# Kernel optimization log

Measured on AMD Instinct MI355X. Metric: run time of the kernel, lower is better.

Reference implementation:

```python
import jax, jax.numpy as jnp
import numpy as np

IN_F = 4096
OUT_F = 4096
BATCH = 4096


def _dequantize(q, mn, mx):
    # Faithful to dequantize_to_float32: per-tensor affine using the *observed*
    # integer min/max of the stored tensor.
    q_min = q.min()
    q_max = q.max()
    scale = (mx - mn) / (q_max - q_min).astype(jnp.float32)
    return (q - q_min).astype(jnp.float32) * scale + mn


def setup_inputs() -> dict:
    key = jax.random.key(0)
    k1, k2, k3 = jax.random.split(key, 3)
    x = jax.random.normal(k1, (BATCH, IN_F), dtype=jnp.float32)
    # int8-valued weights/bias stored as int32 (same math; dequant uses tensor min/max)
    weight_q = jax.random.randint(k2, (OUT_F, IN_F), -128, 128, dtype=jnp.int32)
    bias_q = jax.random.randint(k3, (OUT_F,), -128, 128, dtype=jnp.int32)
    # per-tensor float range recorded at quantization time (original scales by 255 first,
    # so these ranges are on the scaled tensor; any floats work for correctness testing)
    weight_min = jnp.float32(-4.2)
    weight_max = jnp.float32(4.5)
    bias_min = jnp.float32(-1.3)
    bias_max = jnp.float32(1.1)
    return {
        "x": x,
        "weight_q": weight_q,
        "bias_q": bias_q,
        "weight_min": weight_min,
        "weight_max": weight_max,
        "bias_min": bias_min,
        "bias_max": bias_max,
    }


def reference(x, weight_q, bias_q, weight_min, weight_max, bias_min, bias_max):
    w = _dequantize(weight_q, weight_min, weight_max)   # [OUT_F, IN_F] fp32
    b = _dequantize(bias_q, bias_min, bias_max)         # [OUT_F] fp32
    # F.linear: x @ W^T + b
    return jnp.einsum("bi,oi->bo", x, w) + b
```

## Files before the change

kernel.cpp:

```cpp
#include <hip/hip_runtime.h>
#include <climits>

#define IN_F 4096
#define OUT_F 4096
#define BATCH 4096
#define NPART 1024

typedef __bf16 bf16x8 __attribute__((ext_vector_type(8)));
typedef float f32x4 __attribute__((ext_vector_type(4)));

__device__ __forceinline__ unsigned short f2bf_rne(float f) {
  unsigned int u = __float_as_uint(f);
  u += 0x7fffu + ((u >> 16) & 1u);
  return (unsigned short)(u >> 16);
}

__global__ __launch_bounds__(256) void k_conv(const float* __restrict__ x,
                                              const int* __restrict__ q,
                                              unsigned short* __restrict__ xb,
                                              unsigned short* __restrict__ qb,
                                              float* __restrict__ rowsum,
                                              int* __restrict__ pmin,
                                              int* __restrict__ pmax) {
  if (blockIdx.x < NPART) {
    const int n4 = (OUT_F * IN_F) / 4;
    const int stride = NPART * 256;
    int vmin = INT_MAX, vmax = INT_MIN;
    const int4* q4 = (const int4*)q;
    ushort4* qb4 = (ushort4*)qb;
    for (int i = blockIdx.x * 256 + threadIdx.x; i < n4; i += stride) {
      int4 v = q4[i];
      vmin = min(vmin, min(min(v.x, v.y), min(v.z, v.w)));
      vmax = max(vmax, max(max(v.x, v.y), max(v.z, v.w)));
      ushort4 h;
      h.x = f2bf_rne((float)v.x);
      h.y = f2bf_rne((float)v.y);
      h.z = f2bf_rne((float)v.z);
      h.w = f2bf_rne((float)v.w);
      qb4[i] = h;
    }
    for (int off = 32; off > 0; off >>= 1) {
      vmin = min(vmin, __shfl_down(vmin, off));
      vmax = max(vmax, __shfl_down(vmax, off));
    }
    __shared__ int rmin[4], rmax[4];
    const int wave = threadIdx.x >> 6;
    if ((threadIdx.x & 63) == 0) { rmin[wave] = vmin; rmax[wave] = vmax; }
    __syncthreads();
    if (threadIdx.x == 0) {
      pmin[blockIdx.x] = min(min(rmin[0], rmin[1]), min(rmin[2], rmin[3]));
      pmax[blockIdx.x] = max(max(rmax[0], rmax[1]), max(rmax[2], rmax[3]));
    }
  } else {
    const int wave = threadIdx.x >> 6;
    const int lane = threadIdx.x & 63;
    const int row = (blockIdx.x - NPART) * 4 + wave;
    const float4* xr = (const float4*)(x + (size_t)row * IN_F);
    ushort4* xbr = (ushort4*)(xb + (size_t)row * IN_F);
    float s = 0.f;
#pragma unroll
    for (int it = 0; it < IN_F / 4 / 64; ++it) {
      const int i = it * 64 + lane;
      float4 v = xr[i];
      s += (v.x + v.y) + (v.z + v.w);
      ushort4 h;
      h.x = f2bf_rne(v.x); h.y = f2bf_rne(v.y);
      h.z = f2bf_rne(v.z); h.w = f2bf_rne(v.w);
      xbr[i] = h;
    }
    for (int off = 32; off > 0; off >>= 1) s += __shfl_down(s, off);
    if (lane == 0) rowsum[row] = s;
  }
}

__global__ __launch_bounds__(256) void k_wmm(const int* __restrict__ q,
                                             int* __restrict__ pmin,
                                             int* __restrict__ pmax) {
  const int n4 = (OUT_F * IN_F) / 4;
  const int stride = gridDim.x * blockDim.x;
  int vmin = INT_MAX, vmax = INT_MIN;
  const int4* q4 = (const int4*)q;
  for (int i = blockIdx.x * blockDim.x + threadIdx.x; i < n4; i += stride) {
    int4 v = q4[i];
    vmin = min(vmin, min(min(v.x, v.y), min(v.z, v.w)));
    vmax = max(vmax, max(max(v.x, v.y), max(v.z, v.w)));
  }
  for (int off = 32; off > 0; off >>= 1) {
    vmin = min(vmin, __shfl_down(vmin, off));
    vmax = max(vmax, __shfl_down(vmax, off));
  }
  __shared__ int rmin[4], rmax[4];
  const int wave = threadIdx.x >> 6;
  if ((threadIdx.x & 63) == 0) { rmin[wave] = vmin; rmax[wave] = vmax; }
  __syncthreads();
  if (threadIdx.x == 0) {
    pmin[blockIdx.x] = min(min(rmin[0], rmin[1]), min(rmin[2], rmin[3]));
    pmax[blockIdx.x] = max(max(rmax[0], rmax[1]), max(rmax[2], rmax[3]));
  }
}

__global__ __launch_bounds__(256) void k_scal(const int* __restrict__ pmin,
                                              const int* __restrict__ pmax, int npart,
                                              const int* __restrict__ bq,
                                              const float* __restrict__ wmn,
                                              const float* __restrict__ wmx,
                                              const float* __restrict__ bmn,
                                              const float* __restrict__ bmx,
                                              float* __restrict__ scal) {
  int vmin = INT_MAX, vmax = INT_MIN;
  for (int i = threadIdx.x; i < npart; i += 256) {
    vmin = min(vmin, pmin[i]);
    vmax = max(vmax, pmax[i]);
  }
  int bmin = INT_MAX, bmaxv = INT_MIN;
  for (int i = threadIdx.x; i < OUT_F; i += 256) {
    int v = bq[i];
    bmin = min(bmin, v);
    bmaxv = max(bmaxv, v);
  }
  for (int off = 32; off > 0; off >>= 1) {
    vmin = min(vmin, __shfl_down(vmin, off));
    vmax = max(vmax, __shfl_down(vmax, off));
    bmin = min(bmin, __shfl_down(bmin, off));
    bmaxv = max(bmaxv, __shfl_down(bmaxv, off));
  }
  __shared__ int r[4][4];
  const int wave = threadIdx.x >> 6;
  if ((threadIdx.x & 63) == 0) {
    r[wave][0] = vmin; r[wave][1] = vmax; r[wave][2] = bmin; r[wave][3] = bmaxv;
  }
  __syncthreads();
  if (threadIdx.x == 0) {
    int qmin = min(min(r[0][0], r[1][0]), min(r[2][0], r[3][0]));
    int qmax = max(max(r[0][1], r[1][1]), max(r[2][1], r[3][1]));
    int qbmin = min(min(r[0][2], r[1][2]), min(r[2][2], r[3][2]));
    int qbmax = max(max(r[0][3], r[1][3]), max(r[2][3], r[3][3]));
    float ws = (*wmx - *wmn) / (float)(qmax - qmin);
    scal[0] = ws;
    scal[1] = *wmn - ws * (float)qmin;
    float bs = (*bmx - *bmn) / (float)(qbmax - qbmin);
    scal[2] = bs;
    scal[3] = *bmn - bs * (float)qbmin;
  }
}

__device__ __forceinline__ void load_lds16(const unsigned short* g, unsigned short* l) {
  __builtin_amdgcn_global_load_lds(
      (const __attribute__((address_space(1))) unsigned int*)g,
      (__attribute__((address_space(3))) unsigned int*)l, 16, 0, 0);
}

__global__ __launch_bounds__(256, 3) void k_gemm(
    const unsigned short* __restrict__ A,
    const unsigned short* __restrict__ B,
    const int* __restrict__ bq,
    const float* __restrict__ rowsum,
    const float* __restrict__ scal,
    float* __restrict__ C) {
  __shared__ unsigned short As[128 * 32];
  __shared__ unsigned short Bs[128 * 32];

  const int tid = threadIdx.x;
  const int wave = tid >> 6;
  const int lane = tid & 63;
  const int bm = blockIdx.x * 128;
  const int bn = blockIdx.y * 128;

  const int wm = (wave & 1) * 64;
  const int wn = (wave >> 1) * 64;
  const int row16 = lane & 15;
  const int quad = lane >> 4;

  const int c0 = wave * 2;
  const int r0 = c0 * 16 + (lane >> 2);
  const int r1 = r0 + 16;
  const int ccol = ((lane & 3) ^ ((lane >> 3) & 3)) * 8;
  const unsigned short* Ap0 = A + (size_t)(bm + r0) * IN_F + ccol;
  const unsigned short* Ap1 = A + (size_t)(bm + r1) * IN_F + ccol;
  const unsigned short* Bp0 = B + (size_t)(bn + r0) * IN_F + ccol;
  const unsigned short* Bp1 = B + (size_t)(bn + r1) * IN_F + ccol;
  unsigned short* As0 = &As[c0 * 512];
  unsigned short* As1 = &As[(c0 + 1) * 512];
  unsigned short* Bs0 = &Bs[c0 * 512];
  unsigned short* Bs1 = &Bs[(c0 + 1) * 512];

  const int cread = (quad ^ ((lane >> 1) & 3)) * 8;

  f32x4 acc[4][4] = {};

  for (int k0 = 0; k0 < IN_F; k0 += 32) {
    load_lds16(Ap0 + k0, As0);
    load_lds16(Ap1 + k0, As1);
    load_lds16(Bp0 + k0, Bs0);
    load_lds16(Bp1 + k0, Bs1);
    __syncthreads();

    bf16x8 af[4], bfr[4];
#pragma unroll
    for (int i = 0; i < 4; ++i)
      af[i] = *(const bf16x8*)&As[(wm + i * 16 + row16) * 32 + cread];
#pragma unroll
    for (int i = 0; i < 4; ++i)
      bfr[i] = *(const bf16x8*)&Bs[(wn + i * 16 + row16) * 32 + cread];
#pragma unroll
    for (int mi = 0; mi < 4; ++mi)
#pragma unroll
      for (int ni = 0; ni < 4; ++ni)
        acc[mi][ni] = __builtin_amdgcn_mfma_f32_16x16x32_bf16(af[mi], bfr[ni], acc[mi][ni], 0, 0, 0);

    __syncthreads();
  }

  const float wsc = scal[0], wbe = scal[1], bsc = scal[2], bbe = scal[3];
#pragma unroll
  for (int ni = 0; ni < 4; ++ni) {
    const int gn = bn + wn + ni * 16 + row16;
    const float bdq = bsc * (float)bq[gn] + bbe;
#pragma unroll
    for (int mi = 0; mi < 4; ++mi) {
      const int gm0 = bm + wm + mi * 16 + quad * 4;
#pragma unroll
      for (int r = 0; r < 4; ++r) {
        const int gm = gm0 + r;
        C[(size_t)gm * OUT_F + gn] = wsc * acc[mi][ni][r] + wbe * rowsum[gm] + bdq;
      }
    }
  }
}

__global__ void k_naive(const float* __restrict__ x, const int* __restrict__ wq,
                        const int* __restrict__ bq, const float* __restrict__ scal,
                        float* __restrict__ out) {
  const int o = blockIdx.x * blockDim.x + threadIdx.x;
  const int b = blockIdx.y;
  const float* xr = x + (size_t)b * IN_F;
  const int* wr = wq + (size_t)o * IN_F;
  float s = 0.f, sx = 0.f;
  for (int k = 0; k < IN_F; ++k) {
    float xv = xr[k];
    s += xv * (float)wr[k];
    sx += xv;
  }
  out[(size_t)b * OUT_F + o] =
      scal[0] * s + scal[1] * sx + scal[2] * (float)bq[o] + scal[3];
}

extern "C" void kernel_launch(void* const* d_in, const int* in_sizes, int n_in,
                              void* d_out, int out_size, void* d_ws, size_t ws_size,
                              hipStream_t stream) {
  const float* x = (const float*)d_in[0];
  const int* wq = (const int*)d_in[1];
  const int* bq = (const int*)d_in[2];
  const float* wmn = (const float*)d_in[3];
  const float* wmx = (const float*)d_in[4];
  const float* bmn = (const float*)d_in[5];
  const float* bmx = (const float*)d_in[6];
  float* out = (float*)d_out;

  char* ws = (char*)d_ws;
  float* scal = (float*)ws;
  int* pmin = (int*)(ws + 64);
  int* pmax = (int*)(ws + 64 + NPART * 4);
  float* rowsum = (float*)(ws + 64 + 2 * NPART * 4);
  unsigned short* xb = (unsigned short*)(ws + 32768);
  unsigned short* qb = xb + (size_t)BATCH * IN_F;
  const size_t needed = 32768 + (size_t)BATCH * IN_F * 2 + (size_t)OUT_F * IN_F * 2;

  if (ws_size >= needed) {
    k_conv<<<2 * NPART, 256, 0, stream>>>(x, wq, xb, qb, rowsum, pmin, pmax);
    k_scal<<<1, 256, 0, stream>>>(pmin, pmax, NPART, bq, wmn, wmx, bmn, bmx, scal);
    dim3 grid(BATCH / 128, OUT_F / 128);
    k_gemm<<<grid, 256, 0, stream>>>(xb, qb, bq, rowsum, scal, out);
  } else {
    k_wmm<<<NPART, 256, 0, stream>>>(wq, pmin, pmax);
    k_scal<<<1, 256, 0, stream>>>(pmin, pmax, NPART, bq, wmn, wmx, bmn, bmx, scal);
    k_naive<<<dim3(OUT_F / 256, BATCH), 256, 0, stream>>>(x, wq, bq, scal, out);
  }
}
```

Baseline: 353.9 us.

## Use 256x256 tiles with 8 waves and 4-stage LDS prefetch pipeline

Grows the GEMM block tile from 128x128 to 256x256 with 512 threads. Each wave computes a 128x64 sub-tile in two halves. A 4-slot LDS ring buffer, filled by direct global-to-LDS loads three k-steps ahead, replaces the single-buffer load/sync loop, with explicit vmcnt waits, barriers and setprio around the MFMA bursts. The aim is to hide global load latency behind matrix work and raise data reuse per byte loaded. In exchange it uses more LDS (128 KB per block) and more accumulator registers, which limits occupancy, and the hand-tuned barrier and waitcnt scheme is fragile.

```diff
diff --git a/kernel.cpp b/kernel.cpp
--- a/kernel.cpp
+++ b/kernel.cpp
@@ -150,75 +150,115 @@
       (__attribute__((address_space(3))) unsigned int*)l, 16, 0, 0);
 }
 
-__global__ __launch_bounds__(256, 3) void k_gemm(
+__global__ __launch_bounds__(512, 2) void k_gemm(
     const unsigned short* __restrict__ A,
     const unsigned short* __restrict__ B,
     const int* __restrict__ bq,
     const float* __restrict__ rowsum,
     const float* __restrict__ scal,
     float* __restrict__ C) {
-  __shared__ unsigned short As[128 * 32];
-  __shared__ unsigned short Bs[128 * 32];
+  __shared__ __align__(16) unsigned short As[4][8192];
+  __shared__ __align__(16) unsigned short Bs[4][8192];
 
   const int tid = threadIdx.x;
-  const int wave = tid >> 6;
+  const int w = tid >> 6;
   const int lane = tid & 63;
-  const int bm = blockIdx.x * 128;
-  const int bn = blockIdx.y * 128;
-
-  const int wm = (wave & 1) * 64;
-  const int wn = (wave >> 1) * 64;
-  const int row16 = lane & 15;
-  const int quad = lane >> 4;
-
-  const int c0 = wave * 2;
-  const int r0 = c0 * 16 + (lane >> 2);
-  const int r1 = r0 + 16;
-  const int ccol = ((lane & 3) ^ ((lane >> 3) & 3)) * 8;
-  const unsigned short* Ap0 = A + (size_t)(bm + r0) * IN_F + ccol;
-  const unsigned short* Ap1 = A + (size_t)(bm + r1) * IN_F + ccol;
-  const unsigned short* Bp0 = B + (size_t)(bn + r0) * IN_F + ccol;
-  const unsigned short* Bp1 = B + (size_t)(bn + r1) * IN_F + ccol;
-  unsigned short* As0 = &As[c0 * 512];
-  unsigned short* As1 = &As[(c0 + 1) * 512];
-  unsigned short* Bs0 = &Bs[c0 * 512];
-  unsigned short* Bs1 = &Bs[(c0 + 1) * 512];
-
-  const int cread = (quad ^ ((lane >> 1) & 3)) * 8;
-
-  f32x4 acc[4][4] = {};
-
-  for (int k0 = 0; k0 < IN_F; k0 += 32) {
-    load_lds16(Ap0 + k0, As0);
-    load_lds16(Ap1 + k0, As1);
-    load_lds16(Bp0 + k0, Bs0);
-    load_lds16(Bp1 + k0, Bs1);
-    __syncthreads();
-
-    bf16x8 af[4], bfr[4];
+  const int bm = blockIdx.x * 256;
+  const int bn = blockIdx.y * 256;
+
+  const int wm = (w & 1) * 128;
+  const int wn = (w >> 1) * 64;
+  const int r16 = lane & 15;
+  const int q = lane >> 4;
+  const int pc = (q ^ ((r16 >> 1) & 3)) * 8;
+
+  const int cA0 = w * 128 + lane;
+  const int rowS0 = cA0 >> 2;
+  const int colS0 = ((cA0 & 3) ^ ((rowS0 >> 1) & 3)) * 8;
+  const int cA1 = cA0 + 64;
+  const int rowS1 = cA1 >> 2;
+  const int colS1 = ((cA1 & 3) ^ ((rowS1 >> 1) & 3)) * 8;
+  const unsigned short* srcA0 = A + (size_t)(bm + rowS0) * IN_F + colS0;
+  const unsigned short* srcA1 = A + (size_t)(bm + rowS1) * IN_F + colS1;
+  const unsigned short* srcB0 = B + (size_t)(bn + rowS0) * IN_F + colS0;
+  const unsigned short* srcB1 = B + (size_t)(bn + rowS1) * IN_F + colS1;
+  const int dst0 = w * 1024;
+  const int dst1 = w * 1024 + 512;
+
+  f32x4 acc[8][4] = {};
+
+  const int NT = IN_F / 32;
+
+#pragma unroll
+  for (int t = 0; t < 3; ++t) {
+    load_lds16(srcA0 + t * 32, &As[t][dst0]);
+    load_lds16(srcA1 + t * 32, &As[t][dst1]);
+    load_lds16(srcB0 + t * 32, &Bs[t][dst0]);
+    load_lds16(srcB1 + t * 32, &Bs[t][dst1]);
+  }
+  asm volatile("s_waitcnt vmcnt(8)" ::: "memory");
+  __builtin_amdgcn_s_barrier();
+
+  for (int t = 0; t < NT; ++t) {
+    const int s = t & 3;
+    const unsigned short* Asl = As[s];
+    const unsigned short* Bsl = Bs[s];
+    const int s3 = (t + 3) & 3;
+    const int koff = (t + 3) * 32;
+    const bool pf = (t + 3 < NT);
+
+    bf16x8 afr[4], bfr[4];
 #pragma unroll
     for (int i = 0; i < 4; ++i)
-      af[i] = *(const bf16x8*)&As[(wm + i * 16 + row16) * 32 + cread];
+      afr[i] = *(const bf16x8*)&Asl[(wm + i * 16 + r16) * 32 + pc];
 #pragma unroll
     for (int i = 0; i < 4; ++i)
-      bfr[i] = *(const bf16x8*)&Bs[(wn + i * 16 + row16) * 32 + cread];
+      bfr[i] = *(const bf16x8*)&Bsl[(wn + i * 16 + r16) * 32 + pc];
+    if (pf) {
+      load_lds16(srcA0 + koff, &As[s3][dst0]);
+      load_lds16(srcA1 + koff, &As[s3][dst1]);
+    }
+    __builtin_amdgcn_s_barrier();
+    __builtin_amdgcn_s_setprio(1);
 #pragma unroll
     for (int mi = 0; mi < 4; ++mi)
 #pragma unroll
       for (int ni = 0; ni < 4; ++ni)
-        acc[mi][ni] = __builtin_amdgcn_mfma_f32_16x16x32_bf16(af[mi], bfr[ni], acc[mi][ni], 0, 0, 0);
-
-    __syncthreads();
+        acc[mi][ni] = __builtin_amdgcn_mfma_f32_16x16x32_bf16(afr[mi], bfr[ni], acc[mi][ni], 0, 0, 0);
+    __builtin_amdgcn_s_setprio(0);
+    __builtin_amdgcn_s_barrier();
+
+    bf16x8 af2[4];
+#pragma unroll
+    for (int i = 0; i < 4; ++i)
+      af2[i] = *(const bf16x8*)&Asl[(wm + 64 + i * 16 + r16) * 32 + pc];
+    if (pf) {
+      load_lds16(srcB0 + koff, &Bs[s3][dst0]);
+      load_lds16(srcB1 + koff, &Bs[s3][dst1]);
+    }
+    __builtin_amdgcn_s_barrier();
+    __builtin_amdgcn_s_setprio(1);
+#pragma unroll
+    for (int mi = 0; mi < 4; ++mi)
+#pragma unroll
+      for (int ni = 0; ni < 4; ++ni)
+        acc[4 + mi][ni] = __builtin_amdgcn_mfma_f32_16x16x32_bf16(af2[mi], bfr[ni], acc[4 + mi][ni], 0, 0, 0);
+    __builtin_amdgcn_s_setprio(0);
+
+    if (t < NT - 3)       asm volatile("s_waitcnt vmcnt(8)" ::: "memory");
+    else if (t == NT - 3) asm volatile("s_waitcnt vmcnt(4)" ::: "memory");
+    else if (t == NT - 2) asm volatile("s_waitcnt vmcnt(0)" ::: "memory");
+    __builtin_amdgcn_s_barrier();
   }
 
   const float wsc = scal[0], wbe = scal[1], bsc = scal[2], bbe = scal[3];
 #pragma unroll
   for (int ni = 0; ni < 4; ++ni) {
-    const int gn = bn + wn + ni * 16 + row16;
+    const int gn = bn + wn + ni * 16 + r16;
     const float bdq = bsc * (float)bq[gn] + bbe;
 #pragma unroll
-    for (int mi = 0; mi < 4; ++mi) {
-      const int gm0 = bm + wm + mi * 16 + quad * 4;
+    for (int mi = 0; mi < 8; ++mi) {
+      const int gm0 = bm + wm + mi * 16 + q * 4;
 #pragma unroll
       for (int r = 0; r < 4; ++r) {
         const int gm = gm0 + r;
@@ -269,8 +309,8 @@
   if (ws_size >= needed) {
     k_conv<<<2 * NPART, 256, 0, stream>>>(x, wq, xb, qb, rowsum, pmin, pmax);
     k_scal<<<1, 256, 0, stream>>>(pmin, pmax, NPART, bq, wmn, wmx, bmn, bmx, scal);
-    dim3 grid(BATCH / 128, OUT_F / 128);
-    k_gemm<<<grid, 256, 0, stream>>>(xb, qb, bq, rowsum, scal, out);
+    dim3 grid(BATCH / 256, OUT_F / 256);
+    k_gemm<<<grid, 512, 0, stream>>>(xb, qb, bq, rowsum, scal, out);
   } else {
     k_wmm<<<NPART, 256, 0, stream>>>(wq, pmin, pmax);
     k_scal<<<1, 256, 0, stream>>>(pmin, pmax, NPART, bq, wmn, wmx, bmn, bmx, scal);
```

Result: faster. 318.8 us (-9.9%).
